# Performance work log

Hardware: AMD Instinct MI355X
Metric: run time of the kernel (lower is better)

Reference implementation:

```python
import jax, jax.numpy as jnp
import numpy as np

B, T, C, H = 2, 2048, 1024, 16
D = C // H  # 64
RW, RA, RG = 64, 64, 128  # decay / a / gate LoRA ranks
EPS = 1e-5


def setup_inputs() -> dict:
    key = jax.random.key(0)
    ks = iter(jax.random.split(key, 40))
    n = lambda s, sc=0.02: jax.random.normal(next(ks), s, jnp.float32) * sc
    u = lambda s: jax.random.uniform(next(ks), s, jnp.float32)
    return dict(
        hidden_states=jax.random.normal(next(ks), (B, T, C), jnp.float32),
        # token-mix (time-shift lerp) params
        x_r=u((C,)), x_w=u((C,)), x_k=u((C,)), x_v=u((C,)), x_a=u((C,)), x_g=u((C,)),
        k_k=u((C,)), k_a=u((C,)), r_k=n((H, D), 0.1),
        # square projections (stored [in, out]; x @ W)
        W_r=n((C, C)), W_k=n((C, C)), W_v=n((C, C)), W_o=n((C, C)),
        # LoRA: out = act(x @ A) @ Bm + bias (activation between the two linears)
        w_lora_a=n((C, RW)), w_lora_b=n((RW, C)), w_lora_bias=n((C,), 0.1),
        a_lora_a=n((C, RA)), a_lora_b=n((RA, C)), a_lora_bias=jnp.zeros((C,), jnp.float32),
        g_lora_a=n((C, RG)), g_lora_b=n((RG, C)), g_lora_bias=jnp.zeros((C,), jnp.float32),
        # GroupNorm(num_heads groups over value_dim)
        gn_weight=jnp.ones((C,), jnp.float32), gn_bias=jnp.zeros((C,), jnp.float32),
    )


def _rwkv7_scan(r, log_w, k, v, a, b):
    # all inputs [B, T, H, D]; state S: [B, H, D_v, D_k]
    # S_t = S_{t-1} * diag(exp(log_w_t)) + (S_{t-1} @ a_t) b_t^T + v_t k_t^T
    # o_t = S_t @ r_t
    Bn, Tn, Hn, Dn = r.shape

    def step(S, xs):
        r_t, w_t, k_t, v_t, a_t, b_t = xs  # each [B, H, D]
        sa = jnp.einsum('bhij,bhj->bhi', S, a_t)          # S @ a (pre-decay state)
        S = (S * jnp.exp(w_t)[:, :, None, :]
             + sa[..., None] * b_t[:, :, None, :]
             + v_t[..., None] * k_t[:, :, None, :])
        o_t = jnp.einsum('bhij,bhj->bhi', S, r_t)
        return S, o_t

    S0 = jnp.zeros((Bn, Hn, Dn, Dn), r.dtype)
    xs = tuple(jnp.swapaxes(x, 0, 1) for x in (r, log_w, k, v, a, b))  # [T,B,H,D]
    _, o = jax.lax.scan(step, S0, xs)
    return jnp.swapaxes(o, 0, 1)  # [B, T, H, D]


def reference(hidden_states, x_r, x_w, x_k, x_v, x_a, x_g, k_k, k_a, r_k,
              W_r, W_k, W_v, W_o,
              w_lora_a, w_lora_b, w_lora_bias,
              a_lora_a, a_lora_b, a_lora_bias,
              g_lora_a, g_lora_b, g_lora_bias,
              gn_weight, gn_bias):
    Bn, Tn, Cn = hidden_states.shape
    # time shift: pad one step of zeros at the front, drop last
    shifted = jnp.concatenate([jnp.zeros_like(hidden_states[:, :1]), hidden_states[:, :-1]], axis=1)
    delta = shifted - hidden_states

    xr = hidden_states + delta * x_r
    xw = hidden_states + delta * x_w
    xk = hidden_states + delta * x_k
    xv = hidden_states + delta * x_v
    xa = hidden_states + delta * x_a

    r = xr @ W_r
    log_w = -jax.nn.softplus(-((jnp.tanh(xw @ w_lora_a) @ w_lora_b) + w_lora_bias)) - 0.5
    k = xk @ W_k
    v = xv @ W_v
    a = jax.nn.sigmoid((xa @ a_lora_a) @ a_lora_b + a_lora_bias)
    # g_lora(r): sigmoid activation sits BETWEEN the two LoRA linears
    g = jax.nn.sigmoid(r @ g_lora_a) @ g_lora_b + g_lora_bias

    kk = (k * k_k).reshape(Bn, Tn, H, D)
    kk = kk / jnp.maximum(jnp.linalg.norm(kk, axis=-1, keepdims=True), 1e-12)  # per-head L2 norm
    k = k * (1.0 + (a - 1.0) * k_a)

    rh = r.reshape(Bn, Tn, H, D)
    wh = log_w.reshape(Bn, Tn, H, D)
    kh = k.reshape(Bn, Tn, H, D)
    vh = v.reshape(Bn, Tn, H, D)
    ah = a.reshape(Bn, Tn, H, D)

    o = _rwkv7_scan(rh, wh, kh, vh, -kk, kk * ah)  # [B, T, H, D]

    # GroupNorm over value_dim with H groups (stats per head)
    mu = o.mean(-1, keepdims=True)
    var = ((o - mu) ** 2).mean(-1, keepdims=True)
    o_flat = ((o - mu) * jax.lax.rsqrt(var + EPS)).reshape(Bn, Tn, C) * gn_weight + gn_bias

    bonus = ((rh * kh * r_k).sum(-1, keepdims=True) * vh).reshape(Bn, Tn, C)
    o_flat = o_flat + bonus
    return (o_flat * g) @ W_o
```

## Files before the change

kernel.cpp:

```cpp
#include <hip/hip_runtime.h>
#include <hip/hip_bf16.h>
#include <hip/hip_fp16.h>
#include <stdint.h>
#include <stddef.h>

typedef __hip_bfloat16 bf16;
typedef _Float16 f16;
typedef __attribute__((ext_vector_type(8))) short short8;
typedef __attribute__((ext_vector_type(8))) _Float16 half8;
typedef __attribute__((ext_vector_type(4))) float f32x4;
typedef __attribute__((ext_vector_type(2))) float f32x2;
typedef unsigned short us;

__device__ __forceinline__ float dsigm(float z){ return 1.f/(1.f+expf(-z)); }

template<int CTRL>
__device__ __forceinline__ float dpp_term(float x) {
  int xi = __builtin_bit_cast(int, x);
  int yi = __builtin_amdgcn_update_dpp(0, xi, CTRL, 0xF, 0xF, false);
  return __builtin_bit_cast(float, yi);
}
__device__ __forceinline__ float red8(float x) {
  x += dpp_term<0xB1>(x);
  x += dpp_term<0x4E>(x);
  x += dpp_term<0x141>(x);
  return x;
}

__device__ __forceinline__ void split1(float v, us& h, us& l) {
  bf16 hb = __float2bfloat16(v);
  h = __builtin_bit_cast(us, hb);
  float hf = __bfloat162float(hb);
  bf16 lb = __float2bfloat16(v - hf);
  l = __builtin_bit_cast(us, lb);
}

__device__ __forceinline__ void split8(const float* f, short8& h, short8& l) {
#pragma unroll
  for (int e = 0; e < 8; ++e) {
    us hh, ll;
    split1(f[e], hh, ll);
    h[e] = (short)hh; l[e] = (short)ll;
  }
}

__device__ __forceinline__ void gl16(const f16* g, f16* l) {
  __builtin_amdgcn_global_load_lds((const __attribute__((address_space(1))) void*)g,
                                   (__attribute__((address_space(3))) void*)l, 16, 0, 0);
}

__device__ __forceinline__ void emit16(const float* __restrict__ marr, int c4,
    const float4& cur, const float4& dlt, f16* __restrict__ out, int row)
{
  float4 m = *(const float4*)(marr + c4);
  f16* o = out + (size_t)row*1024 + c4;
  o[0] = (f16)fmaf(dlt.x, m.x, cur.x);
  o[1] = (f16)fmaf(dlt.y, m.y, cur.y);
  o[2] = (f16)fmaf(dlt.z, m.z, cur.z);
  o[3] = (f16)fmaf(dlt.w, m.w, cur.w);
}

__global__ void k_prep(const float* __restrict__ hs,
    const float* __restrict__ mr, const float* __restrict__ mw, const float* __restrict__ mk,
    const float* __restrict__ mv, const float* __restrict__ ma,
    f16* __restrict__ oxr, f16* __restrict__ oxw, f16* __restrict__ oxk,
    f16* __restrict__ oxv, f16* __restrict__ oxa)
{
  int id = blockIdx.x * 256 + threadIdx.x;
  int row = id >> 8;
  int c4 = (id & 255) << 2;
  int t = row & 2047;
  const float* hp = hs + (size_t)row*1024 + c4;
  float4 cur = *(const float4*)hp;
  float4 prev = make_float4(0.f,0.f,0.f,0.f);
  if (t > 0) prev = *(const float4*)(hp - 1024);
  float4 dlt = make_float4(prev.x-cur.x, prev.y-cur.y, prev.z-cur.z, prev.w-cur.w);
  emit16(mr, c4, cur, dlt, oxr, row);
  emit16(mw, c4, cur, dlt, oxw, row);
  emit16(mk, c4, cur, dlt, oxk, row);
  emit16(mv, c4, cur, dlt, oxv, row);
  emit16(ma, c4, cur, dlt, oxa, row);
}

struct SrcP { const float* p[10]; };
struct DstP { f16* p[10]; };

__global__ void k_transpose(SrcP S, DstP Dd)
{
  static constexpr int TR[10]  = {1024,1024,1024,1024,1024,  64,1024,  64,1024, 128};
  static constexpr int TCC[10] = {1024,1024,1024,1024,  64,1024,  64,1024, 128,1024};
  static constexpr int TCP[10] = {1024,1024,1024,1024, 128,1024, 128,1024, 128,1024};
  int z = blockIdx.z;
  int R = TR[z], Cc = TCC[z], Cp = TCP[z];
  int n0 = blockIdx.x * 32, r0 = blockIdx.y * 32;
  if (n0 >= Cp || r0 >= R) return;
  const float* src = S.p[z];
  f16* dst = Dd.p[z];
  int tx = threadIdx.x, ty = threadIdx.y;
  __shared__ float tile[32][33];
  if (n0 < Cc) {
#pragma unroll
    for (int i = 0; i < 4; ++i)
      tile[ty + 8*i][tx] = src[(size_t)(r0 + ty + 8*i)*Cc + n0 + tx];
    __syncthreads();
#pragma unroll
    for (int i = 0; i < 4; ++i)
      dst[(size_t)(n0 + ty + 8*i)*R + r0 + tx] = (f16)tile[tx][ty + 8*i];
  } else {
#pragma unroll
    for (int i = 0; i < 4; ++i)
      dst[(size_t)(n0 + ty + 8*i)*R + r0 + tx] = (f16)0.f;
  }
}

struct GJob {
  const f16* A;
  const f16* Bt;
  float* C;
  f16* Cpk;
  const float* bias;
  int K; int N; int Npk; int ldc; int act;
  int lda; int ldb;
};
struct GJobs { GJob j[5]; };

__global__ __launch_bounds__(256) void k_gemm_fp16(GJobs jobs)
{
  GJob jb = jobs.j[blockIdx.z];
  const int colBase = blockIdx.y * 128;
  if (colBase >= jb.N) return;
  const int rowBase = blockIdx.x * 128;
  __shared__ __align__(16) f16 As[128*64];
  __shared__ __align__(16) f16 Bs[128*64];
  const int tid = threadIdx.x;
  const int l = tid & 63, w = tid >> 6;
  const int wm = w >> 1, wn = w & 1;
  const int lrow = l & 15;
  const int nk = jb.K >> 6;

  const f16* Arow[4]; const f16* Brow[4]; int ld[4];
#pragma unroll
  for (int i2 = 0; i2 < 4; ++i2) {
    int s = (i2*4 + w)*64 + l;
    int ar = s >> 3;
    int unit = s & 7;
    int acs = (unit ^ (ar & 7)) * 8;
    Arow[i2] = jb.A  + (size_t)(rowBase + ar)*jb.lda + acs;
    Brow[i2] = jb.Bt + (size_t)(colBase + ar)*jb.ldb + acs;
    ld[i2] = (i2*4 + w) * 512;
  }

  f32x4 acc[4][4];
#pragma unroll
  for (int i = 0; i < 4; ++i)
#pragma unroll
    for (int j = 0; j < 4; ++j) { f32x4 z = {0.f,0.f,0.f,0.f}; acc[i][j] = z; }

  for (int kt = 0; kt < nk; ++kt) {
    const int kh = kt*64;
#pragma unroll
    for (int i2 = 0; i2 < 4; ++i2) {
      gl16(Arow[i2] + kh, &As[ld[i2]]);
      gl16(Brow[i2] + kh, &Bs[ld[i2]]);
    }
    __syncthreads();
#pragma unroll
    for (int ks = 0; ks < 2; ++ks) {
      half8 ah[4], bh[4];
#pragma unroll
      for (int mt = 0; mt < 4; ++mt) {
        int row = wm*64 + mt*16 + lrow;
        int cu = ks*4 + (l >> 4);
        ah[mt] = *(const half8*)&As[row*64 + ((cu ^ (row & 7)) * 8)];
      }
#pragma unroll
      for (int nt = 0; nt < 4; ++nt) {
        int row = wn*64 + nt*16 + lrow;
        int cu = ks*4 + (l >> 4);
        bh[nt] = *(const half8*)&Bs[row*64 + ((cu ^ (row & 7)) * 8)];
      }
#pragma unroll
      for (int mt = 0; mt < 4; ++mt)
#pragma unroll
        for (int nt = 0; nt < 4; ++nt)
          acc[mt][nt] = __builtin_amdgcn_mfma_f32_16x16x32_f16(ah[mt], bh[nt], acc[mt][nt], 0, 0, 0);
    }
    __syncthreads();
  }
#pragma unroll
  for (int mt = 0; mt < 4; ++mt) {
    int row = rowBase + wm*64 + mt*16 + (l >> 4)*4;
#pragma unroll
    for (int nt = 0; nt < 4; ++nt) {
      int col = colBase + wn*64 + nt*16 + (l & 15);
      float bv = (jb.bias != nullptr) ? jb.bias[col] : 0.f;
#pragma unroll
      for (int rg = 0; rg < 4; ++rg) {
        float v = acc[mt][nt][rg] + bv;
        if (jb.act == 1)      v = dsigm(v);
        else if (jb.act == 2) v = tanhf(v);
        else if (jb.act == 3) v = 0.60653066f * dsigm(v);
        if (jb.C) jb.C[(size_t)(row + rg)*jb.ldc + col] = v;
        if (jb.Cpk && col < jb.Npk)
          jb.Cpk[(size_t)(row + rg)*jb.Npk + col] = (f16)v;
      }
    }
  }
}

__global__ void k_scanprep(f16* __restrict__ kA, f16* __restrict__ aA,
                           const float* __restrict__ kkw, const float* __restrict__ kaw,
                           f16* __restrict__ kkA)
{
  int idx = blockIdx.x * 256 + threadIdx.x;
  size_t gt8 = (size_t)idx * 8;
  int ch = (int)(gt8 & 1023);
  half8 k8 = *(const half8*)(kA + gt8);
  half8 a8 = *(const half8*)(aA + gt8);
  float kw[8], ka_[8];
  *(float4*)&kw[0]  = *(const float4*)(kkw + ch);
  *(float4*)&kw[4]  = *(const float4*)(kkw + ch + 4);
  *(float4*)&ka_[0] = *(const float4*)(kaw + ch);
  *(float4*)&ka_[4] = *(const float4*)(kaw + ch + 4);
  float kkv[8]; float ss = 0.f;
#pragma unroll
  for (int e = 0; e < 8; ++e) { kkv[e] = (float)k8[e] * kw[e]; ss += kkv[e]*kkv[e]; }
  ss += __shfl_xor(ss, 1); ss += __shfl_xor(ss, 2); ss += __shfl_xor(ss, 4);
  float inv = 1.f / fmaxf(sqrtf(ss), 1e-12f);
  half8 kkn8, bb8, kup8;
#pragma unroll
  for (int e = 0; e < 8; ++e) {
    float kkn = kkv[e] * inv;
    float av = (float)a8[e];
    kkn8[e] = (f16)kkn;
    bb8[e]  = (f16)(kkn * av);
    kup8[e] = (f16)((float)k8[e] * fmaf(av - 1.f, ka_[e], 1.f));
  }
  *(half8*)(kkA + gt8) = kkn8;
  *(half8*)(aA + gt8)  = bb8;
  *(half8*)(kA + gt8)  = kup8;
}

__device__ __forceinline__ void step_pk(const float* __restrict__ sb, int s,
    f32x2* u2, f32x2* p2, float* __restrict__ o0A, float* __restrict__ zA,
    size_t base, int i, int q, int j0)
{
  f32x2 ew2[4], kk2[4], bb2[4], kv2[4], rr2[4];
#pragma unroll
  for (int hh = 0; hh < 2; ++hh) {
    float4 a0 = *(const float4*)(sb + 0    + s*64 + j0 + hh*4);
    float4 a1 = *(const float4*)(sb + 512  + s*64 + j0 + hh*4);
    float4 a2 = *(const float4*)(sb + 1024 + s*64 + j0 + hh*4);
    float4 a3 = *(const float4*)(sb + 1536 + s*64 + j0 + hh*4);
    float4 a4 = *(const float4*)(sb + 2048 + s*64 + j0 + hh*4);
    ew2[hh*2+0] = f32x2{a0.x, a0.y}; ew2[hh*2+1] = f32x2{a0.z, a0.w};
    kk2[hh*2+0] = f32x2{a1.x, a1.y}; kk2[hh*2+1] = f32x2{a1.z, a1.w};
    bb2[hh*2+0] = f32x2{a2.x, a2.y}; bb2[hh*2+1] = f32x2{a2.z, a2.w};
    kv2[hh*2+0] = f32x2{a3.x, a3.y}; kv2[hh*2+1] = f32x2{a3.z, a3.w};
    rr2[hh*2+0] = f32x2{a4.x, a4.y}; rr2[hh*2+1] = f32x2{a4.z, a4.w};
  }
  float vi = sb[2560 + s*64 + i];

  f32x2 uk2 = u2[0]*kk2[0], pk2 = p2[0]*kk2[0];
#pragma unroll
  for (int e = 1; e < 4; ++e) { uk2 += u2[e]*kk2[e]; pk2 += p2[e]*kk2[e]; }
  float uk = red8(uk2.x + uk2.y);
  float pk = red8(pk2.x + pk2.y);
  const f32x2 su2 = {-uk, -uk}, sp2 = {-pk, -pk}, vi2 = {vi, vi};
  f32x2 oo2 = {0.f, 0.f}, zz2 = {0.f, 0.f};
#pragma unroll
  for (int e = 0; e < 4; ++e) {
    f32x2 uu = u2[e]*ew2[e] + su2*bb2[e] + vi2*kv2[e];
    u2[e] = uu; oo2 += uu*rr2[e];
    f32x2 pp = p2[e]*ew2[e] + sp2*bb2[e];
    p2[e] = pp; zz2 += pp*rr2[e];
  }
  float oo = red8(oo2.x + oo2.y);
  float zz = red8(zz2.x + zz2.y);
  if (q == 0) { o0A[base + i] = oo; zA[base + i] = zz; }
}

__global__ __launch_bounds__(512) void k_scan_p1(
    const f16* __restrict__ rA, const f16* __restrict__ ewA,
    const f16* __restrict__ kA, const f16* __restrict__ vA,
    const f16* __restrict__ kkA, const f16* __restrict__ bbA,
    float* __restrict__ o0A, float* __restrict__ zA,
    float* __restrict__ UcA, float* __restrict__ PTcA)
{
  const int blk = blockIdx.x;
  const int bh = blk & 31, c = blk >> 5;
  const int b = bh >> 4, h = bh & 15;
  const int tid = threadIdx.x;
  const int i = tid >> 3, q = tid & 7, j0 = q * 8;
  const size_t base0 = (size_t)b*2048*1024 + (size_t)h*64 + (size_t)(c*64)*1024;

  __shared__ __align__(16) float smem[6144];

  const int active = (tid < 384);
  const int a0 = tid >> 6, rm0 = tid & 63, s0 = rm0 >> 3, f0 = rm0 & 7;
  const f16* pa0 = (a0==0) ? ewA : (a0==1) ? kkA : (a0==2) ? bbA :
                   (a0==3) ? kA  : (a0==4) ? rA  : vA;
  const f16* src0 = pa0 + base0 + (size_t)s0*1024 + f0*8;
  const int dst0 = a0*512 + s0*64 + f0*8;

  f32x2 u2[4], p2[4];
#pragma unroll
  for (int e = 0; e < 4; ++e) {
    u2[e] = f32x2{0.f, 0.f};
    float p0 = (j0 + 2*e     == i) ? 1.f : 0.f;
    float p1 = (j0 + 2*e + 1 == i) ? 1.f : 0.f;
    p2[e] = f32x2{p0, p1};
  }

  if (active) {
    half8 hh = *(const half8*)(src0);
    float4 lo = {(float)hh[0], (float)hh[1], (float)hh[2], (float)hh[3]};
    float4 hi = {(float)hh[4], (float)hh[5], (float)hh[6], (float)hh[7]};
    *(float4*)&smem[dst0]     = lo;
    *(float4*)&smem[dst0 + 4] = hi;
  }
  __syncthreads();

  int curb = 0;
  for (int g = 0; g < 8; ++g) {
    half8 n0;
    if (g < 7 && active) n0 = *(const half8*)(src0 + (size_t)(g+1)*8192);
    const float* sb = smem + curb*3072;
#pragma unroll
    for (int s = 0; s < 8; ++s)
      step_pk(sb, s, u2, p2, o0A, zA, base0 + (size_t)(g*8 + s)*1024, i, q, j0);
    if (g < 7 && active) {
      float4 lo = {(float)n0[0], (float)n0[1], (float)n0[2], (float)n0[3]};
      float4 hi = {(float)n0[4], (float)n0[5], (float)n0[6], (float)n0[7]};
      *(float4*)&smem[(curb^1)*3072 + dst0]     = lo;
      *(float4*)&smem[(curb^1)*3072 + dst0 + 4] = hi;
    }
    __syncthreads();
    curb ^= 1;
  }

  const size_t cbase = ((size_t)(bh*32 + c)) * 4096;
  *(float4*)(UcA + cbase + (size_t)i*64 + j0)     = make_float4(u2[0].x,u2[0].y,u2[1].x,u2[1].y);
  *(float4*)(UcA + cbase + (size_t)i*64 + j0 + 4) = make_float4(u2[2].x,u2[2].y,u2[3].x,u2[3].y);
  float (*lds)[65] = (float(*)[65])smem;
#pragma unroll
  for (int e = 0; e < 4; ++e) {
    lds[i][j0 + 2*e]     = p2[e].x;
    lds[i][j0 + 2*e + 1] = p2[e].y;
  }
  __syncthreads();
  float4 w0 = make_float4(lds[j0+0][i], lds[j0+1][i], lds[j0+2][i], lds[j0+3][i]);
  float4 w1 = make_float4(lds[j0+4][i], lds[j0+5][i], lds[j0+6][i], lds[j0+7][i]);
  *(float4*)(PTcA + cbase + (size_t)i*64 + j0)     = w0;
  *(float4*)(PTcA + cbase + (size_t)i*64 + j0 + 4) = w1;
}

__device__ __forceinline__ void chain_body(int c, int bh, int w, int lr, int lq,
    float (&Slds)[64][65], f32x4 (&acc)[4],
    float (&u_c)[4][4], float4 (&p_c)[2][2],
    float (&u_n)[4][4], float4 (&p_n)[2][2],
    const float* __restrict__ UcA, const float* __restrict__ PTcA,
    float* __restrict__ S0A)
{
  const size_t s0base = ((size_t)bh*32 + c) * 4096;
#pragma unroll
  for (int mt = 0; mt < 4; ++mt)
#pragma unroll
    for (int rg = 0; rg < 4; ++rg) {
      Slds[mt*16 + lq*4 + rg][w*16 + lr] = acc[mt][rg];
      if (c > 0) S0A[s0base + (size_t)(mt*16 + lq*4 + rg)*64 + w*16 + lr] = acc[mt][rg];
    }
  __syncthreads();
  if (c + 1 < 32) {
    const size_t nbase = ((size_t)bh*32 + c + 1) * 4096;
#pragma unroll
    for (int mt = 0; mt < 4; ++mt)
#pragma unroll
      for (int rg = 0; rg < 4; ++rg)
        u_n[mt][rg] = UcA[nbase + (size_t)(mt*16 + lq*4 + rg)*64 + w*16 + lr];
#pragma unroll
    for (int kt = 0; kt < 2; ++kt)
#pragma unroll
      for (int hh = 0; hh < 2; ++hh)
        p_n[kt][hh] = *(const float4*)(PTcA + nbase + (size_t)(w*16 + lr)*64 + kt*32 + lq*8 + hh*4);
  }
  short8 pbh[2], pbl[2];
#pragma unroll
  for (int kt = 0; kt < 2; ++kt) {
    float f[8] = {p_c[kt][0].x, p_c[kt][0].y, p_c[kt][0].z, p_c[kt][0].w,
                  p_c[kt][1].x, p_c[kt][1].y, p_c[kt][1].z, p_c[kt][1].w};
    split8(f, pbh[kt], pbl[kt]);
  }
  f32x4 nacc[4];
#pragma unroll
  for (int mt = 0; mt < 4; ++mt) {
    f32x4 z = {u_c[mt][0], u_c[mt][1], u_c[mt][2], u_c[mt][3]};
    nacc[mt] = z;
  }
#pragma unroll
  for (int kt = 0; kt < 2; ++kt)
#pragma unroll
    for (int mt = 0; mt < 4; ++mt) {
      float f[8];
#pragma unroll
      for (int e = 0; e < 8; ++e) f[e] = Slds[mt*16 + lr][kt*32 + lq*8 + e];
      short8 sah, sal;
      split8(f, sah, sal);
      nacc[mt] = __builtin_amdgcn_mfma_f32_16x16x32_bf16(sah, pbh[kt], nacc[mt], 0, 0, 0);
      nacc[mt] = __builtin_amdgcn_mfma_f32_16x16x32_bf16(sal, pbh[kt], nacc[mt], 0, 0, 0);
      nacc[mt] = __builtin_amdgcn_mfma_f32_16x16x32_bf16(sah, pbl[kt], nacc[mt], 0, 0, 0);
    }
#pragma unroll
  for (int mt = 0; mt < 4; ++mt) acc[mt] = nacc[mt];
  __syncthreads();
}

__global__ __launch_bounds__(256) void k_chain(
    const float* __restrict__ UcA, const float* __restrict__ PTcA,
    float* __restrict__ S0A)
{
  const int bh = blockIdx.x;
  const int l = threadIdx.x & 63, w = threadIdx.x >> 6;
  const int lr = l & 15, lq = l >> 4;
  __shared__ float Slds[64][65];

  f32x4 acc[4];
#pragma unroll
  for (int mt = 0; mt < 4; ++mt) { f32x4 z = {0.f,0.f,0.f,0.f}; acc[mt] = z; }

  float u0[4][4], u1[4][4];
  float4 p0[2][2], p1[2][2];
  {
    const size_t cbase = (size_t)bh * 32 * 4096;
#pragma unroll
    for (int mt = 0; mt < 4; ++mt)
#pragma unroll
      for (int rg = 0; rg < 4; ++rg)
        u0[mt][rg] = UcA[cbase + (size_t)(mt*16 + lq*4 + rg)*64 + w*16 + lr];
#pragma unroll
    for (int kt = 0; kt < 2; ++kt)
#pragma unroll
      for (int hh = 0; hh < 2; ++hh)
        p0[kt][hh] = *(const float4*)(PTcA + cbase + (size_t)(w*16 + lr)*64 + kt*32 + lq*8 + hh*4);
  }
  for (int c = 0; c < 32; c += 2) {
    chain_body(c,     bh, w, lr, lq, Slds, acc, u0, p0, u1, p1, UcA, PTcA, S0A);
    chain_body(c + 1, bh, w, lr, lq, Slds, acc, u1, p1, u0, p0, UcA, PTcA, S0A);
  }
}

__global__ __launch_bounds__(256) void k_corrpost(
    const float* __restrict__ S0A, const float* __restrict__ zA,
    const float* __restrict__ o0A, const f16* __restrict__ rA,
    const f16* __restrict__ kA, const f16* __restrict__ vA,
    const float* __restrict__ rk, const float* __restrict__ gnw,
    const float* __restrict__ gnb, const f16* __restrict__ gA,
    f16* __restrict__ yH)
{
  const int blk = blockIdx.x;
  const int bh = blk & 31;
  const int c  = blk >> 5;
  const int b = bh >> 4, h = bh & 15;
  const int l = threadIdx.x & 63, w = threadIdx.x >> 6;
  const int lr = l & 15, lq = l >> 4;

  f32x4 a2[4];
#pragma unroll
  for (int nt = 0; nt < 4; ++nt) { f32x4 z = {0.f,0.f,0.f,0.f}; a2[nt] = z; }

  if (c > 0) {
    const size_t s0base = ((size_t)bh*32 + c) * 4096;
    short8 sbh[4][2], sbl[4][2];
#pragma unroll
    for (int nt = 0; nt < 4; ++nt)
#pragma unroll
      for (int kt = 0; kt < 2; ++kt) {
        float f[8];
#pragma unroll
        for (int e = 0; e < 8; ++e)
          f[e] = S0A[s0base + (size_t)(nt*16 + lr)*64 + kt*32 + lq*8 + e];
        split8(f, sbh[nt][kt], sbl[nt][kt]);
      }
    short8 zh[2], zl[2];
#pragma unroll
    for (int kt = 0; kt < 2; ++kt) {
      const float* zp = zA + ((size_t)(b*2048 + c*64 + w*16 + lr)*16 + h)*64 + kt*32 + lq*8;
      float f[8];
#pragma unroll
      for (int e = 0; e < 8; ++e) f[e] = zp[e];
      split8(f, zh[kt], zl[kt]);
    }
#pragma unroll
    for (int kt = 0; kt < 2; ++kt)
#pragma unroll
      for (int nt = 0; nt < 4; ++nt) {
        a2[nt] = __builtin_amdgcn_mfma_f32_16x16x32_bf16(zh[kt], sbh[nt][kt], a2[nt], 0, 0, 0);
        a2[nt] = __builtin_amdgcn_mfma_f32_16x16x32_bf16(zl[kt], sbh[nt][kt], a2[nt], 0, 0, 0);
        a2[nt] = __builtin_amdgcn_mfma_f32_16x16x32_bf16(zh[kt], sbl[nt][kt], a2[nt], 0, 0, 0);
      }
  }

#pragma unroll
  for (int rg = 0; rg < 4; ++rg) {
    const int tl = w*16 + lq*4 + rg;
    const size_t trow = (size_t)(b*2048 + c*64 + tl);
    const size_t rb = trow*1024 + h*64;
    float o4[4], v4[4];
    float sum = 0.f, pr = 0.f;
#pragma unroll
    for (int nt = 0; nt < 4; ++nt) {
      const int ii = nt*16 + lr;
      float o = o0A[rb + ii] + a2[nt][rg];
      o4[nt] = o; sum += o;
      v4[nt] = (float)vA[rb + ii];
      pr += (float)rA[rb + ii] * (float)kA[rb + ii] * rk[h*64 + ii];
    }
    sum += __shfl_xor(sum,1); sum += __shfl_xor(sum,2);
    sum += __shfl_xor(sum,4); sum += __shfl_xor(sum,8);
    pr  += __shfl_xor(pr,1);  pr  += __shfl_xor(pr,2);
    pr  += __shfl_xor(pr,4);  pr  += __shfl_xor(pr,8);
    float mean = sum * (1.f/64.f);
    float vp = 0.f;
#pragma unroll
    for (int nt = 0; nt < 4; ++nt) { float d = o4[nt]-mean; vp += d*d; }
    vp += __shfl_xor(vp,1); vp += __shfl_xor(vp,2);
    vp += __shfl_xor(vp,4); vp += __shfl_xor(vp,8);
    float inv = rsqrtf(vp*(1.f/64.f) + 1e-5f);
#pragma unroll
    for (int nt = 0; nt < 4; ++nt) {
      const int ii = nt*16 + lr;
      const int ch = h*64 + ii;
      float y = (o4[nt]-mean)*inv*gnw[ch] + gnb[ch];
      y = fmaf(pr, v4[nt], y);
      y *= (float)gA[rb + ii];
      yH[trow*1024 + ch] = (f16)y;
    }
  }
}

extern "C" void kernel_launch(void* const* d_in, const int* in_sizes, int n_in,
                              void* d_out, int out_size, void* d_ws, size_t ws_size,
                              hipStream_t stream)
{
  (void)in_sizes; (void)n_in; (void)out_size; (void)ws_size;
  const float* hs     = (const float*)d_in[0];
  const float* x_r    = (const float*)d_in[1];
  const float* x_w    = (const float*)d_in[2];
  const float* x_k    = (const float*)d_in[3];
  const float* x_v    = (const float*)d_in[4];
  const float* x_a    = (const float*)d_in[5];
  const float* k_k    = (const float*)d_in[7];
  const float* k_a    = (const float*)d_in[8];
  const float* r_k    = (const float*)d_in[9];
  const float* W_r    = (const float*)d_in[10];
  const float* W_k    = (const float*)d_in[11];
  const float* W_v    = (const float*)d_in[12];
  const float* W_o    = (const float*)d_in[13];
  const float* wla    = (const float*)d_in[14];
  const float* wlb    = (const float*)d_in[15];
  const float* wlbias = (const float*)d_in[16];
  const float* ala    = (const float*)d_in[17];
  const float* alb    = (const float*)d_in[18];
  const float* albias = (const float*)d_in[19];
  const float* gla    = (const float*)d_in[20];
  const float* glb    = (const float*)d_in[21];
  const float* glbias = (const float*)d_in[22];
  const float* gnw    = (const float*)d_in[23];
  const float* gnb    = (const float*)d_in[24];

  char* ws = (char*)d_ws;
  size_t cur = 0;
  auto take = [&](size_t bytes) { size_t o = cur; cur += (bytes + 255) & ~(size_t)255; return o; };

  f16* xr_h = (f16*)(ws + take((size_t)4096*1024*2));
  f16* xw_h = (f16*)(ws + take((size_t)4096*1024*2));
  f16* xk_h = (f16*)(ws + take((size_t)4096*1024*2));
  f16* xv_h = (f16*)(ws + take((size_t)4096*1024*2));
  f16* xa_h = (f16*)(ws + take((size_t)4096*1024*2));
  f16* Wr_p  = (f16*)(ws + take((size_t)1024*1024*2));
  f16* Wk_p  = (f16*)(ws + take((size_t)1024*1024*2));
  f16* Wv_p  = (f16*)(ws + take((size_t)1024*1024*2));
  f16* Wo_p  = (f16*)(ws + take((size_t)1024*1024*2));
  f16* wla_p = (f16*)(ws + take((size_t)128*1024*2));
  f16* wlb_p = (f16*)(ws + take((size_t)1024*64*2));
  f16* ala_p = (f16*)(ws + take((size_t)128*1024*2));
  f16* alb_p = (f16*)(ws + take((size_t)1024*64*2));
  f16* gla_p = (f16*)(ws + take((size_t)128*1024*2));
  f16* glb_p = (f16*)(ws + take((size_t)1024*128*2));
  f16* r_h  = (f16*)(ws + take((size_t)4096*1024*2));
  f16* k_h  = (f16*)(ws + take((size_t)4096*1024*2));
  f16* v_h  = (f16*)(ws + take((size_t)4096*1024*2));
  f16* kk_h = (f16*)(ws + take((size_t)4096*1024*2));
  f16* g_h  = (f16*)(ws + take((size_t)4096*1024*2));
  f16* t2w  = (f16*)(ws + take((size_t)4096*64*2));
  f16* t2a  = (f16*)(ws + take((size_t)4096*64*2));
  f16* t2g  = (f16*)(ws + take((size_t)4096*128*2));
  float* z_f  = (float*)(ws + take((size_t)4096*1024*4));
  float* Uc_f = (float*)(ws + take((size_t)4096*1024*4));
  float* PT_f = (float*)(ws + take((size_t)4096*1024*4));
  f16*   ew_h = xw_h;
  f16*   a_h  = xa_h;
  f16*   y_h  = xr_h;
  float* S0_f = (float*)xk_h;
  float* oF   = (float*)d_out;

  k_prep<<<4096, 256, 0, stream>>>(hs, x_r, x_w, x_k, x_v, x_a,
                                   xr_h, xw_h, xk_h, xv_h, xa_h);
  SrcP sp; DstP dp;
  sp.p[0]=W_r; sp.p[1]=W_k; sp.p[2]=W_v; sp.p[3]=W_o;
  sp.p[4]=wla; sp.p[5]=wlb; sp.p[6]=ala; sp.p[7]=alb; sp.p[8]=gla; sp.p[9]=glb;
  dp.p[0]=Wr_p; dp.p[1]=Wk_p; dp.p[2]=Wv_p; dp.p[3]=Wo_p;
  dp.p[4]=wla_p; dp.p[5]=wlb_p; dp.p[6]=ala_p; dp.p[7]=alb_p; dp.p[8]=gla_p; dp.p[9]=glb_p;
  k_transpose<<<dim3(32,32,10), dim3(32,8), 0, stream>>>(sp, dp);

  GJobs J{};
  auto job = [](const f16* A, const f16* Bt, float* C, f16* Cpk, const float* bias,
                int K, int N, int Npk, int ldc, int act, int lda, int ldb) {
    GJob j; j.A=A; j.Bt=Bt; j.C=C; j.Cpk=Cpk; j.bias=bias;
    j.K=K; j.N=N; j.Npk=Npk; j.ldc=ldc; j.act=act; j.lda=lda; j.ldb=ldb;
    return j;
  };

  J.j[0] = job(xr_h, Wr_p,  nullptr, r_h, nullptr, 1024, 1024, 1024, 0, 0, 1024, 1024);
  J.j[1] = job(xk_h, Wk_p,  nullptr, k_h, nullptr, 1024, 1024, 1024, 0, 0, 1024, 1024);
  J.j[2] = job(xv_h, Wv_p,  nullptr, v_h, nullptr, 1024, 1024, 1024, 0, 0, 1024, 1024);
  J.j[3] = job(xw_h, wla_p, nullptr, t2w, nullptr, 1024, 128,  64,   0, 2, 1024, 1024);
  J.j[4] = job(xa_h, ala_p, nullptr, t2a, nullptr, 1024, 128,  64,   0, 0, 1024, 1024);
  k_gemm_fp16<<<dim3(32,8,5), 256, 0, stream>>>(J);

  J = GJobs{};
  J.j[0] = job(t2w, wlb_p, nullptr, ew_h, wlbias, 64,   1024, 1024, 0, 3, 64,   64);
  J.j[1] = job(t2a, alb_p, nullptr, a_h,  albias, 64,   1024, 1024, 0, 1, 64,   64);
  J.j[2] = job(r_h, gla_p, nullptr, t2g,  nullptr, 1024, 128,  128,  0, 1, 1024, 1024);
  k_gemm_fp16<<<dim3(32,8,3), 256, 0, stream>>>(J);

  J = GJobs{};
  J.j[0] = job(t2g, glb_p, nullptr, g_h, glbias, 128, 1024, 1024, 0, 0, 128, 128);
  k_gemm_fp16<<<dim3(32,8,1), 256, 0, stream>>>(J);

  k_scanprep<<<2048, 256, 0, stream>>>(k_h, a_h, k_k, k_a, kk_h);

  k_scan_p1<<<1024, 512, 0, stream>>>(r_h, ew_h, k_h, v_h, kk_h, a_h, oF, z_f, Uc_f, PT_f);
  k_chain<<<32, 256, 0, stream>>>(Uc_f, PT_f, S0_f);

  k_corrpost<<<1024, 256, 0, stream>>>(S0_f, z_f, oF, r_h, k_h, v_h,
                                       r_k, gnw, gnb, g_h, y_h);

  J = GJobs{};
  J.j[0] = job(y_h, Wo_p, (float*)d_out, nullptr, nullptr, 1024, 1024, 0, 1024, 0, 1024, 1024);
  k_gemm_fp16<<<dim3(32,8,1), 256, 0, stream>>>(J);
}
```

Measured before the change: 322.8 us.

## Halve scan chunk block size, give each thread sixteen state columns

The chunked scan kernel now uses 256 threads per block, with each thread owning 16 columns of a state row instead of 8. The cross-lane reductions shrink from 8 lanes to 4, which removes one DPP step per reduction, and each thread loads the shared-memory step inputs in four float4 chunks. The cost is twice as many registers per thread for the u/p state and half as many threads per block, which may lower latency hiding. Loading of the staged inputs is remapped so all 256 threads load four arrays and the first 128 also load r and v.

```diff
diff --git a/kernel.cpp b/kernel.cpp
--- a/kernel.cpp
+++ b/kernel.cpp
@@ -20,10 +20,9 @@
   int yi = __builtin_amdgcn_update_dpp(0, xi, CTRL, 0xF, 0xF, false);
   return __builtin_bit_cast(float, yi);
 }
-__device__ __forceinline__ float red8(float x) {
+__device__ __forceinline__ float red4(float x) {
   x += dpp_term<0xB1>(x);
   x += dpp_term<0x4E>(x);
-  x += dpp_term<0x141>(x);
   return x;
 }
 
@@ -241,46 +240,50 @@
   *(half8*)(kA + gt8)  = kup8;
 }
 
-__device__ __forceinline__ void step_pk(const float* __restrict__ sb, int s,
+__device__ __forceinline__ void step_pk16(const float* __restrict__ sb, int s,
     f32x2* u2, f32x2* p2, float* __restrict__ o0A, float* __restrict__ zA,
     size_t base, int i, int q, int j0)
 {
-  f32x2 ew2[4], kk2[4], bb2[4], kv2[4], rr2[4];
-#pragma unroll
-  for (int hh = 0; hh < 2; ++hh) {
-    float4 a0 = *(const float4*)(sb + 0    + s*64 + j0 + hh*4);
-    float4 a1 = *(const float4*)(sb + 512  + s*64 + j0 + hh*4);
-    float4 a2 = *(const float4*)(sb + 1024 + s*64 + j0 + hh*4);
-    float4 a3 = *(const float4*)(sb + 1536 + s*64 + j0 + hh*4);
-    float4 a4 = *(const float4*)(sb + 2048 + s*64 + j0 + hh*4);
-    ew2[hh*2+0] = f32x2{a0.x, a0.y}; ew2[hh*2+1] = f32x2{a0.z, a0.w};
+  f32x2 kk2[8];
+#pragma unroll
+  for (int hh = 0; hh < 4; ++hh) {
+    float4 a1 = *(const float4*)(sb + 512 + s*64 + j0 + hh*4);
     kk2[hh*2+0] = f32x2{a1.x, a1.y}; kk2[hh*2+1] = f32x2{a1.z, a1.w};
-    bb2[hh*2+0] = f32x2{a2.x, a2.y}; bb2[hh*2+1] = f32x2{a2.z, a2.w};
-    kv2[hh*2+0] = f32x2{a3.x, a3.y}; kv2[hh*2+1] = f32x2{a3.z, a3.w};
-    rr2[hh*2+0] = f32x2{a4.x, a4.y}; rr2[hh*2+1] = f32x2{a4.z, a4.w};
-  }
+  }
+  f32x2 uk2 = u2[0]*kk2[0], pk2 = p2[0]*kk2[0];
+#pragma unroll
+  for (int e = 1; e < 8; ++e) { uk2 += u2[e]*kk2[e]; pk2 += p2[e]*kk2[e]; }
+  float uk = red4(uk2.x + uk2.y);
+  float pk = red4(pk2.x + pk2.y);
   float vi = sb[2560 + s*64 + i];
-
-  f32x2 uk2 = u2[0]*kk2[0], pk2 = p2[0]*kk2[0];
-#pragma unroll
-  for (int e = 1; e < 4; ++e) { uk2 += u2[e]*kk2[e]; pk2 += p2[e]*kk2[e]; }
-  float uk = red8(uk2.x + uk2.y);
-  float pk = red8(pk2.x + pk2.y);
   const f32x2 su2 = {-uk, -uk}, sp2 = {-pk, -pk}, vi2 = {vi, vi};
   f32x2 oo2 = {0.f, 0.f}, zz2 = {0.f, 0.f};
 #pragma unroll
-  for (int e = 0; e < 4; ++e) {
-    f32x2 uu = u2[e]*ew2[e] + su2*bb2[e] + vi2*kv2[e];
-    u2[e] = uu; oo2 += uu*rr2[e];
-    f32x2 pp = p2[e]*ew2[e] + sp2*bb2[e];
-    p2[e] = pp; zz2 += pp*rr2[e];
-  }
-  float oo = red8(oo2.x + oo2.y);
-  float zz = red8(zz2.x + zz2.y);
+  for (int hh = 0; hh < 4; ++hh) {
+    float4 e4 = *(const float4*)(sb + 0    + s*64 + j0 + hh*4);
+    float4 b4 = *(const float4*)(sb + 1024 + s*64 + j0 + hh*4);
+    float4 k4 = *(const float4*)(sb + 1536 + s*64 + j0 + hh*4);
+    float4 r4 = *(const float4*)(sb + 2048 + s*64 + j0 + hh*4);
+    f32x2 ew0 = {e4.x, e4.y}, ew1 = {e4.z, e4.w};
+    f32x2 bb0 = {b4.x, b4.y}, bb1 = {b4.z, b4.w};
+    f32x2 kv0 = {k4.x, k4.y}, kv1 = {k4.z, k4.w};
+    f32x2 rr0 = {r4.x, r4.y}, rr1 = {r4.z, r4.w};
+    int e0 = hh*2, e1 = hh*2 + 1;
+    f32x2 uu0 = u2[e0]*ew0 + su2*bb0 + vi2*kv0;
+    u2[e0] = uu0; oo2 += uu0*rr0;
+    f32x2 pp0 = p2[e0]*ew0 + sp2*bb0;
+    p2[e0] = pp0; zz2 += pp0*rr0;
+    f32x2 uu1 = u2[e1]*ew1 + su2*bb1 + vi2*kv1;
+    u2[e1] = uu1; oo2 += uu1*rr1;
+    f32x2 pp1 = p2[e1]*ew1 + sp2*bb1;
+    p2[e1] = pp1; zz2 += pp1*rr1;
+  }
+  float oo = red4(oo2.x + oo2.y);
+  float zz = red4(zz2.x + zz2.y);
   if (q == 0) { o0A[base + i] = oo; zA[base + i] = zz; }
 }
 
-__global__ __launch_bounds__(512) void k_scan_p1(
+__global__ __launch_bounds__(256) void k_scan_p1(
     const f16* __restrict__ rA, const f16* __restrict__ ewA,
     const f16* __restrict__ kA, const f16* __restrict__ vA,
     const f16* __restrict__ kkA, const f16* __restrict__ bbA,
@@ -291,68 +294,85 @@
   const int bh = blk & 31, c = blk >> 5;
   const int b = bh >> 4, h = bh & 15;
   const int tid = threadIdx.x;
-  const int i = tid >> 3, q = tid & 7, j0 = q * 8;
+  const int i = tid >> 2, q = tid & 3, j0 = q * 16;
   const size_t base0 = (size_t)b*2048*1024 + (size_t)h*64 + (size_t)(c*64)*1024;
 
   __shared__ __align__(16) float smem[6144];
 
-  const int active = (tid < 384);
-  const int a0 = tid >> 6, rm0 = tid & 63, s0 = rm0 >> 3, f0 = rm0 & 7;
-  const f16* pa0 = (a0==0) ? ewA : (a0==1) ? kkA : (a0==2) ? bbA :
-                   (a0==3) ? kA  : (a0==4) ? rA  : vA;
-  const f16* src0 = pa0 + base0 + (size_t)s0*1024 + f0*8;
-  const int dst0 = a0*512 + s0*64 + f0*8;
-
-  f32x2 u2[4], p2[4];
-#pragma unroll
-  for (int e = 0; e < 4; ++e) {
+  const int aA_ = tid >> 6, rmA = tid & 63, ssA = rmA >> 3, fA = rmA & 7;
+  const f16* paA = (aA_==0) ? ewA : (aA_==1) ? kkA : (aA_==2) ? bbA : kA;
+  const f16* srcA = paA + base0 + (size_t)ssA*1024 + fA*8;
+  const int dstA = aA_*512 + ssA*64 + fA*8;
+  const int hasB = (tid < 128);
+  const int sB = 256 + tid;
+  const int aB_ = sB >> 6, rmB = sB & 63, ssB = rmB >> 3, fB = rmB & 7;
+  const f16* paB = (aB_ == 4) ? rA : vA;
+  const f16* srcB = paB + base0 + (size_t)ssB*1024 + fB*8;
+  const int dstB = aB_*512 + ssB*64 + fB*8;
+
+  f32x2 u2[8], p2[8];
+#pragma unroll
+  for (int e = 0; e < 8; ++e) {
     u2[e] = f32x2{0.f, 0.f};
     float p0 = (j0 + 2*e     == i) ? 1.f : 0.f;
     float p1 = (j0 + 2*e + 1 == i) ? 1.f : 0.f;
     p2[e] = f32x2{p0, p1};
   }
 
-  if (active) {
-    half8 hh = *(const half8*)(src0);
-    float4 lo = {(float)hh[0], (float)hh[1], (float)hh[2], (float)hh[3]};
-    float4 hi = {(float)hh[4], (float)hh[5], (float)hh[6], (float)hh[7]};
-    *(float4*)&smem[dst0]     = lo;
-    *(float4*)&smem[dst0 + 4] = hi;
+  {
+    half8 hA = *(const half8*)(srcA);
+    *(float4*)&smem[dstA]     = make_float4((float)hA[0], (float)hA[1], (float)hA[2], (float)hA[3]);
+    *(float4*)&smem[dstA + 4] = make_float4((float)hA[4], (float)hA[5], (float)hA[6], (float)hA[7]);
+    if (hasB) {
+      half8 hB = *(const half8*)(srcB);
+      *(float4*)&smem[dstB]     = make_float4((float)hB[0], (float)hB[1], (float)hB[2], (float)hB[3]);
+      *(float4*)&smem[dstB + 4] = make_float4((float)hB[4], (float)hB[5], (float)hB[6], (float)hB[7]);
+    }
   }
   __syncthreads();
 
   int curb = 0;
   for (int g = 0; g < 8; ++g) {
-    half8 n0;
-    if (g < 7 && active) n0 = *(const half8*)(src0 + (size_t)(g+1)*8192);
+    half8 nA, nB;
+    if (g < 7) {
+      nA = *(const half8*)(srcA + (size_t)(g+1)*8192);
+      if (hasB) nB = *(const half8*)(srcB + (size_t)(g+1)*8192);
+    }
     const float* sb = smem + curb*3072;
 #pragma unroll
     for (int s = 0; s < 8; ++s)
-      step_pk(sb, s, u2, p2, o0A, zA, base0 + (size_t)(g*8 + s)*1024, i, q, j0);
-    if (g < 7 && active) {
-      float4 lo = {(float)n0[0], (float)n0[1], (float)n0[2], (float)n0[3]};
-      float4 hi = {(float)n0[4], (float)n0[5], (float)n0[6], (float)n0[7]};
-      *(float4*)&smem[(curb^1)*3072 + dst0]     = lo;
-      *(float4*)&smem[(curb^1)*3072 + dst0 + 4] = hi;
+      step_pk16(sb, s, u2, p2, o0A, zA, base0 + (size_t)(g*8 + s)*1024, i, q, j0);
+    if (g < 7) {
+      int nb = curb ^ 1;
+      *(float4*)&smem[nb*3072 + dstA]     = make_float4((float)nA[0], (float)nA[1], (float)nA[2], (float)nA[3]);
+      *(float4*)&smem[nb*3072 + dstA + 4] = make_float4((float)nA[4], (float)nA[5], (float)nA[6], (float)nA[7]);
+      if (hasB) {
+        *(float4*)&smem[nb*3072 + dstB]     = make_float4((float)nB[0], (float)nB[1], (float)nB[2], (float)nB[3]);
+        *(float4*)&smem[nb*3072 + dstB + 4] = make_float4((float)nB[4], (float)nB[5], (float)nB[6], (float)nB[7]);
+      }
     }
     __syncthreads();
     curb ^= 1;
   }
 
   const size_t cbase = ((size_t)(bh*32 + c)) * 4096;
-  *(float4*)(UcA + cbase + (size_t)i*64 + j0)     = make_float4(u2[0].x,u2[0].y,u2[1].x,u2[1].y);
-  *(float4*)(UcA + cbase + (size_t)i*64 + j0 + 4) = make_float4(u2[2].x,u2[2].y,u2[3].x,u2[3].y);
+#pragma unroll
+  for (int e4 = 0; e4 < 4; ++e4)
+    *(float4*)(UcA + cbase + (size_t)i*64 + j0 + e4*4) =
+      make_float4(u2[e4*2].x, u2[e4*2].y, u2[e4*2+1].x, u2[e4*2+1].y);
   float (*lds)[65] = (float(*)[65])smem;
 #pragma unroll
-  for (int e = 0; e < 4; ++e) {
+  for (int e = 0; e < 8; ++e) {
     lds[i][j0 + 2*e]     = p2[e].x;
     lds[i][j0 + 2*e + 1] = p2[e].y;
   }
   __syncthreads();
-  float4 w0 = make_float4(lds[j0+0][i], lds[j0+1][i], lds[j0+2][i], lds[j0+3][i]);
-  float4 w1 = make_float4(lds[j0+4][i], lds[j0+5][i], lds[j0+6][i], lds[j0+7][i]);
-  *(float4*)(PTcA + cbase + (size_t)i*64 + j0)     = w0;
-  *(float4*)(PTcA + cbase + (size_t)i*64 + j0 + 4) = w1;
+#pragma unroll
+  for (int e4 = 0; e4 < 4; ++e4) {
+    float4 wv = make_float4(lds[j0 + e4*4 + 0][i], lds[j0 + e4*4 + 1][i],
+                            lds[j0 + e4*4 + 2][i], lds[j0 + e4*4 + 3][i]);
+    *(float4*)(PTcA + cbase + (size_t)i*64 + j0 + e4*4) = wv;
+  }
 }
 
 __device__ __forceinline__ void chain_body(int c, int bh, int w, int lr, int lq,
@@ -640,7 +660,7 @@
 
   k_scanprep<<<2048, 256, 0, stream>>>(k_h, a_h, k_k, k_a, kk_h);
 
-  k_scan_p1<<<1024, 512, 0, stream>>>(r_h, ew_h, k_h, v_h, kk_h, a_h, oF, z_f, Uc_f, PT_f);
+  k_scan_p1<<<1024, 256, 0, stream>>>(r_h, ew_h, k_h, v_h, kk_h, a_h, oF, z_f, Uc_f, PT_f);
   k_chain<<<32, 256, 0, stream>>>(Uc_f, PT_f, S0_f);
 
   k_corrpost<<<1024, 256, 0, stream>>>(S0_f, z_f, oF, r_h, k_h, v_h,
```

Result: faster. 315.4 us, median of 2 (-2.3%).
